# Performance work log

Hardware: AMD Instinct MI355X
Metric: run time of the kernel (lower is better)

## Reference

```python
import jax, jax.numpy as jnp
import numpy as np

BATCH, SEQ, D_IN, D_H = 128, 256, 1024, 1024


def setup_inputs() -> dict:
    key = jax.random.key(0)
    k = jax.random.split(key, 5)
    s = 0.02  # small init scale, like trained weights
    return {
        "x": jax.random.normal(k[0], (BATCH, SEQ, D_IN), dtype=jnp.float32),
        "W0": jax.random.normal(k[1], (3, D_IN + D_H, D_H), dtype=jnp.float32) * s,
        "b0": jax.random.normal(k[2], (3, D_H), dtype=jnp.float32) * s,
        "W1": jax.random.normal(k[3], (3, 2 * D_H, D_H), dtype=jnp.float32) * s,
        "b1": jax.random.normal(k[4], (3, D_H), dtype=jnp.float32) * s,
    }


def _cell(x, h, W, b):
    # non-standard GRU cell: f,i from concat(x,h); z from concat(x, h*i)
    cat = jnp.concatenate([x, h], axis=-1)            # [B, in+H]
    f = jax.nn.sigmoid(cat @ W[0] + b[0])             # forget-like gate
    i = jax.nn.sigmoid(cat @ W[1] + b[1])             # input gate on h
    z = jnp.tanh(jnp.concatenate([x, h * i], axis=-1) @ W[2] + b[2])
    return (1.0 - f) * h + f * z


def reference(x, W0, b0, W1, b1):
    sg = jax.lax.stop_gradient
    batch = x.shape[0]
    h0 = jnp.zeros((batch, D_H), dtype=x.dtype)

    def step(h, x_t):
        h = _cell(x_t, sg(h), W0, b0)                 # first layer (h detached)
        h = _cell(sg(h), sg(h), W1, b1)               # hidden layer (both detached); dropout p=0 -> identity
        return h, None

    xs = jnp.swapaxes(x, 0, 1)                        # [T, B, D_in]
    h_final, _ = jax.lax.scan(step, h0, xs)
    return h_final
```

## Files before the change

### kernel.cpp

```cpp
#include <hip/hip_runtime.h>

#define BB    128
#define TSEQ  256
#define DH    1024
#define DK2   2048
#define NWG   256
#define NTHR  512

typedef __attribute__((ext_vector_type(8))) short short8;
typedef __attribute__((ext_vector_type(4))) float f32x4;

__device__ __forceinline__ unsigned short f2bf(float f) {
    union { float f; unsigned int u; } v; v.f = f;
    unsigned int r = (v.u + 0x7FFFu + ((v.u >> 16) & 1u)) >> 16;
    return (unsigned short)r;
}

__device__ __forceinline__ int imin2(int a, int b) { return a < b ? a : b; }

#define MFMA(a, b, c) __builtin_amdgcn_mfma_f32_16x16x32_bf16((a), (b), (c), 0, 0, 0)

__device__ __forceinline__ void cstoref(float* p, float v) {
    asm volatile("global_store_dword %0, %1, off sc0 sc1" :: "v"(p), "v"(v) : "memory");
}
__device__ __forceinline__ void cstoreh(unsigned short* p, unsigned short v) {
    unsigned int w = v;
    asm volatile("global_store_short %0, %1, off sc0 sc1" :: "v"(p), "v"(w) : "memory");
}

template<int INV>
__device__ __forceinline__ void gbar(int* bar, int lg, int wg) {
    asm volatile("s_waitcnt vmcnt(0)" ::: "memory");
    __syncthreads();
    const int tid = threadIdx.x;
    if (tid == 0) {
        int* fp = bar + wg * 16;
        int v = lg + 1;
        asm volatile("global_store_dword %0, %1, off sc0 sc1" :: "v"(fp), "v"(v) : "memory");
    }
    if (tid < 64) {
        const int* f0 = bar + (tid +   0) * 16;
        const int* f1 = bar + (tid +  64) * 16;
        const int* f2 = bar + (tid + 128) * 16;
        const int* f3 = bar + (tid + 192) * 16;
        const int target = lg + 1;
        for (;;) {
            int a, b, c, d;
            asm volatile("global_load_dword %0, %1, off sc0 sc1" : "=v"(a) : "v"(f0) : "memory");
            asm volatile("global_load_dword %0, %1, off sc0 sc1" : "=v"(b) : "v"(f1) : "memory");
            asm volatile("global_load_dword %0, %1, off sc0 sc1" : "=v"(c) : "v"(f2) : "memory");
            asm volatile("global_load_dword %0, %1, off sc0 sc1" : "=v"(d) : "v"(f3) : "memory");
            asm volatile("s_waitcnt vmcnt(0)" ::: "memory");
            int m = imin2(imin2(a, b), imin2(c, d));
            #pragma unroll
            for (int off = 32; off >= 1; off >>= 1)
                m = imin2(m, __shfl_xor(m, off, 64));
            if (__builtin_amdgcn_readfirstlane(m) >= target) break;
            __builtin_amdgcn_s_sleep(1);
        }
        if (INV) __builtin_amdgcn_fence(__ATOMIC_ACQUIRE, "agent");
    }
    __syncthreads();
}

__global__ __launch_bounds__(256) void prep_weights(const float* __restrict__ W0,
                                                    const float* __restrict__ W1,
                                                    unsigned short* W0f, unsigned short* W0i,
                                                    unsigned short* W0z, unsigned short* Wff,
                                                    unsigned short* Wii, unsigned short* W1z,
                                                    float* h, unsigned short* hb,
                                                    int* bar) {
    int job = blockIdx.x;
    if (job >= 10240) {
        int i0 = (job - 10240) * 2048 + threadIdx.x;
        #pragma unroll
        for (int k = 0; k < 8; ++k) { int i = i0 + k * 256; h[i] = 0.f; hb[i] = 0; }
        return;
    }
    if (job == 0) {
        for (int i = threadIdx.x; i < 4096; i += 256) bar[i] = 0;
    }
    __shared__ float tl[32][33];
    const int tx = threadIdx.x & 31, ty = threadIdx.x >> 5;
    if (job < 6144) {
        int g = job >> 11, r = job & 2047, kt = r >> 5, nt = r & 31;
        const float* src = W0 + (size_t)g * DK2 * DH;
        unsigned short* dst = (g == 0) ? W0f : ((g == 1) ? W0i : W0z);
        #pragma unroll
        for (int i = 0; i < 4; ++i)
            tl[ty + i * 8][tx] = src[(size_t)(kt * 32 + ty + i * 8) * DH + nt * 32 + tx];
        __syncthreads();
        #pragma unroll
        for (int i = 0; i < 4; ++i)
            dst[(size_t)(nt * 32 + ty + i * 8) * DK2 + kt * 32 + tx] = f2bf(tl[tx][ty + i * 8]);
    } else if (job < 8192) {
        int r = job - 6144; int g = r >> 10; r &= 1023;
        int kt = r >> 5, nt = r & 31;
        const float* src = W1 + (size_t)g * DK2 * DH;
        unsigned short* dst = (g == 0) ? Wff : Wii;
        #pragma unroll
        for (int i = 0; i < 4; ++i)
            tl[ty + i * 8][tx] = src[(size_t)(kt * 32 + ty + i * 8) * DH + nt * 32 + tx]
                               + src[(size_t)(1024 + kt * 32 + ty + i * 8) * DH + nt * 32 + tx];
        __syncthreads();
        #pragma unroll
        for (int i = 0; i < 4; ++i)
            dst[(size_t)(nt * 32 + ty + i * 8) * DH + kt * 32 + tx] = f2bf(tl[tx][ty + i * 8]);
    } else {
        int r = job - 8192; int kt = r >> 5, nt = r & 31;
        const float* src = W1 + (size_t)2 * DK2 * DH;
        #pragma unroll
        for (int i = 0; i < 4; ++i)
            tl[ty + i * 8][tx] = src[(size_t)(kt * 32 + ty + i * 8) * DH + nt * 32 + tx];
        __syncthreads();
        #pragma unroll
        for (int i = 0; i < 4; ++i)
            W1z[(size_t)(nt * 32 + ty + i * 8) * DK2 + kt * 32 + tx] = f2bf(tl[tx][ty + i * 8]);
    }
}

struct GruParams {
    const float* x;
    const float* b0;
    const float* b1;
    const unsigned short* W0f;
    const unsigned short* W0i;
    const unsigned short* W0z;
    const unsigned short* Wff;
    const unsigned short* Wii;
    const unsigned short* W1z;
    float* xpre;
    float* h;  unsigned short* hb;
    float* fg;
    unsigned short* hib;
    float* h1;
    unsigned short* hcat;
    float* f2g;
    float* out;
    int* bar;
};

__global__ __launch_bounds__(NTHR) void gru_main(GruParams P) {
    const int wg   = blockIdx.x;
    const int xcd  = wg & 7;
    const int sub  = wg >> 3;
    const int tid  = threadIdx.x;
    const int lane = tid & 63;
    const int wv   = tid >> 6;
    const int tile = wv & 3, ks2 = wv >> 2;
    const int cw   = wv & 1, ks4 = wv >> 1;
    const int lr   = lane & 15;
    const int kb   = (lane >> 4) * 8;
    const int drow = (lane >> 4) * 4;

    __shared__ float s_red[4][16][17];
    __shared__ float s_r2[2][3][16][17];

    int lg = 0;
    const int band = xcd * 128;

    for (int t = 0; t < TSEQ; ++t) {
        if ((t & 31) == 0) {
            for (int j = sub; j < 192; j += 32) {
                int mb = j / 6, cj = j % 6;
                int g = cj >> 1, off = (cj & 1) * 64;
                int col0 = band + off;
                int b = wv * 16 + lr;
                const float* xp = P.x + ((size_t)b * TSEQ + (t + mb)) * DH + kb;
                const unsigned short* wt = (g == 0) ? P.W0f : ((g == 1) ? P.W0i : P.W0z);
                const unsigned short* wp = wt + (size_t)(col0 + lr) * DK2 + kb;
                f32x4 a0 = {0,0,0,0}, a1 = a0, a2 = a0, a3 = a0;
                #pragma unroll 2
                for (int k = 0; k < DH; k += 32) {
                    f32x4 lo = *(const f32x4*)(xp + k);
                    f32x4 hi = *(const f32x4*)(xp + k + 4);
                    short8 av;
                    av[0] = (short)f2bf(lo[0]); av[1] = (short)f2bf(lo[1]);
                    av[2] = (short)f2bf(lo[2]); av[3] = (short)f2bf(lo[3]);
                    av[4] = (short)f2bf(hi[0]); av[5] = (short)f2bf(hi[1]);
                    av[6] = (short)f2bf(hi[2]); av[7] = (short)f2bf(hi[3]);
                    short8 b0v = *(const short8*)(wp + k);
                    short8 b1v = *(const short8*)(wp + (size_t)16 * DK2 + k);
                    short8 b2v = *(const short8*)(wp + (size_t)32 * DK2 + k);
                    short8 b3v = *(const short8*)(wp + (size_t)48 * DK2 + k);
                    a0 = MFMA(av, b0v, a0);
                    a1 = MFMA(av, b1v, a1);
                    a2 = MFMA(av, b2v, a2);
                    a3 = MFMA(av, b3v, a3);
                }
                int rowb = mb * 128 + wv * 16 + drow;
                #pragma unroll
                for (int cf = 0; cf < 4; ++cf) {
                    f32x4 acc = (cf == 0) ? a0 : ((cf == 1) ? a1 : ((cf == 2) ? a2 : a3));
                    int col = g * DH + col0 + cf * 16 + lr;
                    #pragma unroll
                    for (int rr = 0; rr < 4; ++rr)
                        cstoref(P.xpre + (size_t)(rowb + rr) * 3072 + col, acc[rr]);
                }
            }
            gbar<0>(P.bar, lg, wg); ++lg;
        }
        const int tq = t & 31;

        {
            int gate = sub >> 4, rem = sub & 15;
            int mb = rem >> 2, nbq = rem & 3;
            const unsigned short* wt = gate ? P.W0i : P.W0f;
            int wm = tile >> 1, wn = tile & 1;
            int rowb = mb * 32 + wm * 16, colb = band + nbq * 32 + wn * 16;
            const unsigned short* ap = P.hb + (size_t)(rowb + lr) * DH + ks2 * 512 + kb;
            const unsigned short* wp = wt + (size_t)(colb + lr) * DK2 + 1024 + ks2 * 512 + kb;
            int n = colb + lr;
            short8 a[16];
            #pragma unroll
            for (int k = 0; k < 16; ++k) a[k] = *(const short8*)(ap + (size_t)k * 32);
            float xv[4] = {0,0,0,0}, hv[4] = {0,0,0,0};
            if (ks2 == 0) {
                #pragma unroll
                for (int rr = 0; rr < 4; ++rr)
                    xv[rr] = P.xpre[(size_t)(tq * 128 + rowb + drow + rr) * 3072 + gate * DH + n];
                if (gate == 1) {
                    #pragma unroll
                    for (int rr = 0; rr < 4; ++rr)
                        hv[rr] = P.h[(size_t)(rowb + drow + rr) * DH + n];
                }
            }
            short8 bw[16];
            #pragma unroll
            for (int k = 0; k < 16; ++k) bw[k] = *(const short8*)(wp + (size_t)k * 32);
            f32x4 acc = {0.f, 0.f, 0.f, 0.f};
            #pragma unroll
            for (int k = 0; k < 16; ++k) acc = MFMA(a[k], bw[k], acc);
            if (ks2 == 1) {
                s_red[tile][drow + 0][lr] = acc[0]; s_red[tile][drow + 1][lr] = acc[1];
                s_red[tile][drow + 2][lr] = acc[2]; s_red[tile][drow + 3][lr] = acc[3];
            }
            __syncthreads();
            if (ks2 == 0) {
                acc[0] += s_red[tile][drow + 0][lr]; acc[1] += s_red[tile][drow + 1][lr];
                acc[2] += s_red[tile][drow + 2][lr]; acc[3] += s_red[tile][drow + 3][lr];
                float bias = P.b0[gate * DH + n];
                #pragma unroll
                for (int rr = 0; rr < 4; ++rr) {
                    int b = rowb + drow + rr;
                    float pre = acc[rr] + xv[rr] + bias;
                    float s = 1.f / (1.f + __expf(-pre));
                    if (gate == 0) cstoref(P.fg + (size_t)b * DH + n, s);
                    else           cstoreh(P.hib + (size_t)b * DH + n, f2bf(hv[rr] * s));
                }
            }
            gbar<0>(P.bar, lg, wg); ++lg;
        }

        {
            int rowb = (sub >> 2) * 16, colb = band + (sub & 3) * 32 + cw * 16;
            const unsigned short* ap = P.hib + (size_t)(rowb + lr) * DH + ks4 * 256 + kb;
            const unsigned short* wp = P.W0z + (size_t)(colb + lr) * DK2 + 1024 + ks4 * 256 + kb;
            int n = colb + lr;
            short8 a[8];
            #pragma unroll
            for (int k = 0; k < 8; ++k) a[k] = *(const short8*)(ap + (size_t)k * 32);
            float xv[4] = {0,0,0,0}, fv[4] = {0,0,0,0}, hv[4] = {0,0,0,0};
            if (ks4 == 0) {
                #pragma unroll
                for (int rr = 0; rr < 4; ++rr) {
                    int b = rowb + drow + rr;
                    xv[rr] = P.xpre[(size_t)(tq * 128 + b) * 3072 + 2 * DH + n];
                    fv[rr] = P.fg[(size_t)b * DH + n];
                    hv[rr] = P.h[(size_t)b * DH + n];
                }
            }
            short8 bw[8];
            #pragma unroll
            for (int k = 0; k < 8; ++k) bw[k] = *(const short8*)(wp + (size_t)k * 32);
            f32x4 acc = {0.f, 0.f, 0.f, 0.f};
            #pragma unroll
            for (int k = 0; k < 8; ++k) acc = MFMA(a[k], bw[k], acc);
            if (ks4 != 0) {
                s_r2[cw][ks4 - 1][drow + 0][lr] = acc[0]; s_r2[cw][ks4 - 1][drow + 1][lr] = acc[1];
                s_r2[cw][ks4 - 1][drow + 2][lr] = acc[2]; s_r2[cw][ks4 - 1][drow + 3][lr] = acc[3];
            }
            __syncthreads();
            if (ks4 == 0) {
                #pragma unroll
                for (int rr = 0; rr < 4; ++rr)
                    acc[rr] += s_r2[cw][0][drow + rr][lr] + s_r2[cw][1][drow + rr][lr]
                             + s_r2[cw][2][drow + rr][lr];
                float bias = P.b0[2 * DH + n];
                #pragma unroll
                for (int rr = 0; rr < 4; ++rr) {
                    int b = rowb + drow + rr;
                    float pre = acc[rr] + xv[rr] + bias;
                    float z = tanhf(pre);
                    float nh = (1.f - fv[rr]) * hv[rr] + fv[rr] * z;
                    cstoref(P.h1 + (size_t)b * DH + n, nh);
                    cstoreh(P.hcat + (size_t)b * DK2 + n, f2bf(nh));
                }
            }
            gbar<0>(P.bar, lg, wg); ++lg;
        }

        {
            int gate = sub >> 4, rem = sub & 15;
            int mb = rem >> 2, nbq = rem & 3;
            const unsigned short* wt = gate ? P.Wii : P.Wff;
            int wm = tile >> 1, wn = tile & 1;
            int rowb = mb * 32 + wm * 16, colb = band + nbq * 32 + wn * 16;
            const unsigned short* ap = P.hcat + (size_t)(rowb + lr) * DK2 + ks2 * 512 + kb;
            const unsigned short* wp = wt + (size_t)(colb + lr) * DH + ks2 * 512 + kb;
            int n = colb + lr;
            short8 a[16];
            #pragma unroll
            for (int k = 0; k < 16; ++k) a[k] = *(const short8*)(ap + (size_t)k * 32);
            float h1v[4] = {0,0,0,0};
            if (ks2 == 0 && gate == 1) {
                #pragma unroll
                for (int rr = 0; rr < 4; ++rr)
                    h1v[rr] = P.h1[(size_t)(rowb + drow + rr) * DH + n];
            }
            short8 bw[16];
            #pragma unroll
            for (int k = 0; k < 16; ++k) bw[k] = *(const short8*)(wp + (size_t)k * 32);
            f32x4 acc = {0.f, 0.f, 0.f, 0.f};
            #pragma unroll
            for (int k = 0; k < 16; ++k) acc = MFMA(a[k], bw[k], acc);
            if (ks2 == 1) {
                s_red[tile][drow + 0][lr] = acc[0]; s_red[tile][drow + 1][lr] = acc[1];
                s_red[tile][drow + 2][lr] = acc[2]; s_red[tile][drow + 3][lr] = acc[3];
            }
            __syncthreads();
            if (ks2 == 0) {
                acc[0] += s_red[tile][drow + 0][lr]; acc[1] += s_red[tile][drow + 1][lr];
                acc[2] += s_red[tile][drow + 2][lr]; acc[3] += s_red[tile][drow + 3][lr];
                float bias = P.b1[gate * DH + n];
                #pragma unroll
                for (int rr = 0; rr < 4; ++rr) {
                    int b = rowb + drow + rr;
                    float pre = acc[rr] + bias;
                    float s = 1.f / (1.f + __expf(-pre));
                    if (gate == 0) cstoref(P.f2g + (size_t)b * DH + n, s);
                    else           cstoreh(P.hcat + (size_t)b * DK2 + DH + n, f2bf(h1v[rr] * s));
                }
            }
            gbar<0>(P.bar, lg, wg); ++lg;
        }

        {
            int rowb = (sub >> 2) * 16, colb = band + (sub & 3) * 32 + cw * 16;
            const unsigned short* ap = P.hcat + (size_t)(rowb + lr) * DK2 + ks4 * 512 + kb;
            const unsigned short* wp = P.W1z + (size_t)(colb + lr) * DK2 + ks4 * 512 + kb;
            int n = colb + lr;
            short8 a[16];
            #pragma unroll
            for (int k = 0; k < 16; ++k) a[k] = *(const short8*)(ap + (size_t)k * 32);
            float f2v[4] = {0,0,0,0}, h1v[4] = {0,0,0,0};
            if (ks4 == 0) {
                #pragma unroll
                for (int rr = 0; rr < 4; ++rr) {
                    int b = rowb + drow + rr;
                    f2v[rr] = P.f2g[(size_t)b * DH + n];
                    h1v[rr] = P.h1[(size_t)b * DH + n];
                }
            }
            short8 bw[16];
            #pragma unroll
            for (int k = 0; k < 16; ++k) bw[k] = *(const short8*)(wp + (size_t)k * 32);
            f32x4 acc = {0.f, 0.f, 0.f, 0.f};
            #pragma unroll
            for (int k = 0; k < 16; ++k) acc = MFMA(a[k], bw[k], acc);
            if (ks4 != 0) {
                s_r2[cw][ks4 - 1][drow + 0][lr] = acc[0]; s_r2[cw][ks4 - 1][drow + 1][lr] = acc[1];
                s_r2[cw][ks4 - 1][drow + 2][lr] = acc[2]; s_r2[cw][ks4 - 1][drow + 3][lr] = acc[3];
            }
            __syncthreads();
            if (ks4 == 0) {
                #pragma unroll
                for (int rr = 0; rr < 4; ++rr)
                    acc[rr] += s_r2[cw][0][drow + rr][lr] + s_r2[cw][1][drow + rr][lr]
                             + s_r2[cw][2][drow + rr][lr];
                float bias = P.b1[2 * DH + n];
                #pragma unroll
                for (int rr = 0; rr < 4; ++rr) {
                    int b = rowb + drow + rr;
                    float pre = acc[rr] + bias;
                    float z = tanhf(pre);
                    float nh = (1.f - f2v[rr]) * h1v[rr] + f2v[rr] * z;
                    cstoref(P.h + (size_t)b * DH + n, nh);
                    cstoreh(P.hb + (size_t)b * DH + n, f2bf(nh));
                    if (t == TSEQ - 1) P.out[(size_t)b * DH + n] = nh;
                }
            }
            gbar<1>(P.bar, lg, wg); ++lg;
        }
    }
}

extern "C" void kernel_launch(void* const* d_in, const int* in_sizes, int n_in,
                              void* d_out, int out_size, void* d_ws, size_t ws_size,
                              hipStream_t stream) {
    const float* x  = (const float*)d_in[0];
    const float* W0 = (const float*)d_in[1];
    const float* b0 = (const float*)d_in[2];
    const float* W1 = (const float*)d_in[3];
    const float* b1 = (const float*)d_in[4];

    char* ws = (char*)d_ws;
    size_t off = 0;
    auto alloc = [&](size_t bytes) { void* p = ws + off; off += (bytes + 255) & ~(size_t)255; return p; };

    unsigned short* W0f = (unsigned short*)alloc((size_t)DH * DK2 * 2);
    unsigned short* W0i = (unsigned short*)alloc((size_t)DH * DK2 * 2);
    unsigned short* W0z = (unsigned short*)alloc((size_t)DH * DK2 * 2);
    unsigned short* W1z = (unsigned short*)alloc((size_t)DH * DK2 * 2);
    unsigned short* Wff = (unsigned short*)alloc((size_t)DH * DH * 2);
    unsigned short* Wii = (unsigned short*)alloc((size_t)DH * DH * 2);
    float* xpre = (float*)alloc((size_t)32 * 128 * 3072 * 4);
    float* h    = (float*)alloc((size_t)BB * DH * 4);
    unsigned short* hb = (unsigned short*)alloc((size_t)BB * DH * 2);
    float* fg   = (float*)alloc((size_t)BB * DH * 4);
    unsigned short* hib = (unsigned short*)alloc((size_t)BB * DH * 2);
    float* h1   = (float*)alloc((size_t)BB * DH * 4);
    unsigned short* hcat = (unsigned short*)alloc((size_t)BB * DK2 * 2);
    float* f2g  = (float*)alloc((size_t)BB * DH * 4);
    int* bar    = (int*)alloc(16384);
    (void)ws_size; (void)in_sizes; (void)n_in; (void)out_size;

    prep_weights<<<10304, 256, 0, stream>>>(W0, W1, W0f, W0i, W0z, Wff, Wii, W1z,
                                            h, hb, bar);

    GruParams p;
    p.x = x; p.b0 = b0; p.b1 = b1;
    p.W0f = W0f; p.W0i = W0i; p.W0z = W0z; p.Wff = Wff; p.Wii = Wii; p.W1z = W1z;
    p.xpre = xpre; p.h = h; p.hb = hb; p.fg = fg; p.hib = hib;
    p.h1 = h1; p.hcat = hcat; p.f2g = f2g;
    p.out = (float*)d_out;
    p.bar = bar;

    void* args[] = { &p };
    hipLaunchCooperativeKernel((const void*)gru_main, dim3(NWG), dim3(NTHR), args, 0, stream);
}
```

Measured before the change: 11.62 ms.

## Split batch into independent WG clusters with per-cluster grid barriers

```diff
diff --git a/kernel.cpp b/kernel.cpp
--- a/kernel.cpp
+++ b/kernel.cpp
@@ -39,19 +39,13 @@
         asm volatile("global_store_dword %0, %1, off sc0 sc1" :: "v"(fp), "v"(v) : "memory");
     }
     if (tid < 64) {
-        const int* f0 = bar + (tid +   0) * 16;
-        const int* f1 = bar + (tid +  64) * 16;
-        const int* f2 = bar + (tid + 128) * 16;
-        const int* f3 = bar + (tid + 192) * 16;
+        const int* f0 = bar + ((wg >> 6) * 64 + tid) * 16;
         const int target = lg + 1;
         for (;;) {
-            int a, b, c, d;
+            int a;
             asm volatile("global_load_dword %0, %1, off sc0 sc1" : "=v"(a) : "v"(f0) : "memory");
-            asm volatile("global_load_dword %0, %1, off sc0 sc1" : "=v"(b) : "v"(f1) : "memory");
-            asm volatile("global_load_dword %0, %1, off sc0 sc1" : "=v"(c) : "v"(f2) : "memory");
-            asm volatile("global_load_dword %0, %1, off sc0 sc1" : "=v"(d) : "v"(f3) : "memory");
             asm volatile("s_waitcnt vmcnt(0)" ::: "memory");
-            int m = imin2(imin2(a, b), imin2(c, d));
+            int m = a;
             #pragma unroll
             for (int off = 32; off >= 1; off >>= 1)
                 m = imin2(m, __shfl_xor(m, off, 64));
@@ -142,8 +136,8 @@
 
 __global__ __launch_bounds__(NTHR) void gru_main(GruParams P) {
     const int wg   = blockIdx.x;
-    const int xcd  = wg & 7;
-    const int sub  = wg >> 3;
+    const int c    = wg >> 6;
+    const int cwg  = wg & 63;
     const int tid  = threadIdx.x;
     const int lane = tid & 63;
     const int wv   = tid >> 6;
@@ -157,18 +151,21 @@
     __shared__ float s_r2[2][3][16][17];
 
     int lg = 0;
-    const int band = xcd * 128;
+    const int crow = c * 32;
+
+    const int gateAC = cwg >> 5, nctAC = cwg & 31;
+    const int rhBD   = cwg >> 5, nctBD = cwg & 31;
 
     for (int t = 0; t < TSEQ; ++t) {
         if ((t & 31) == 0) {
-            for (int j = sub; j < 192; j += 32) {
-                int mb = j / 6, cj = j % 6;
-                int g = cj >> 1, off = (cj & 1) * 64;
-                int col0 = band + off;
-                int b = wv * 16 + lr;
-                const float* xp = P.x + ((size_t)b * TSEQ + (t + mb)) * DH + kb;
+            for (int j = cwg; j < 384; j += 64) {
+                int tt = j / 12, cj = j % 12;
+                int g = cj >> 2;
+                int gcol0 = (cj & 3) * 256 + (wv & 3) * 64;
+                int b = crow + (wv >> 2) * 16 + lr;
+                const float* xp = P.x + ((size_t)b * TSEQ + (t + tt)) * DH + kb;
                 const unsigned short* wt = (g == 0) ? P.W0f : ((g == 1) ? P.W0i : P.W0z);
-                const unsigned short* wp = wt + (size_t)(col0 + lr) * DK2 + kb;
+                const unsigned short* wp = wt + (size_t)(gcol0 + lr) * DK2 + kb;
                 f32x4 a0 = {0,0,0,0}, a1 = a0, a2 = a0, a3 = a0;
                 #pragma unroll 2
                 for (int k = 0; k < DH; k += 32) {
@@ -188,11 +185,11 @@
                     a2 = MFMA(av, b2v, a2);
                     a3 = MFMA(av, b3v, a3);
                 }
-                int rowb = mb * 128 + wv * 16 + drow;
+                int rowb = tt * 128 + crow + (wv >> 2) * 16 + drow;
                 #pragma unroll
                 for (int cf = 0; cf < 4; ++cf) {
                     f32x4 acc = (cf == 0) ? a0 : ((cf == 1) ? a1 : ((cf == 2) ? a2 : a3));
-                    int col = g * DH + col0 + cf * 16 + lr;
+                    int col = g * DH + gcol0 + cf * 16 + lr;
                     #pragma unroll
                     for (int rr = 0; rr < 4; ++rr)
                         cstoref(P.xpre + (size_t)(rowb + rr) * 3072 + col, acc[rr]);
@@ -203,11 +200,10 @@
         const int tq = t & 31;
 
         {
-            int gate = sub >> 4, rem = sub & 15;
-            int mb = rem >> 2, nbq = rem & 3;
+            const int gate = gateAC;
             const unsigned short* wt = gate ? P.W0i : P.W0f;
             int wm = tile >> 1, wn = tile & 1;
-            int rowb = mb * 32 + wm * 16, colb = band + nbq * 32 + wn * 16;
+            int rowb = crow + wm * 16, colb = nctAC * 32 + wn * 16;
             const unsigned short* ap = P.hb + (size_t)(rowb + lr) * DH + ks2 * 512 + kb;
             const unsigned short* wp = wt + (size_t)(colb + lr) * DK2 + 1024 + ks2 * 512 + kb;
             int n = colb + lr;
@@ -253,7 +249,7 @@
         }
 
         {
-            int rowb = (sub >> 2) * 16, colb = band + (sub & 3) * 32 + cw * 16;
+            int rowb = crow + rhBD * 16, colb = nctBD * 32 + cw * 16;
             const unsigned short* ap = P.hib + (size_t)(rowb + lr) * DH + ks4 * 256 + kb;
             const unsigned short* wp = P.W0z + (size_t)(colb + lr) * DK2 + 1024 + ks4 * 256 + kb;
             int n = colb + lr;
@@ -301,11 +297,10 @@
         }
 
         {
-            int gate = sub >> 4, rem = sub & 15;
-            int mb = rem >> 2, nbq = rem & 3;
+            const int gate = gateAC;
             const unsigned short* wt = gate ? P.Wii : P.Wff;
             int wm = tile >> 1, wn = tile & 1;
-            int rowb = mb * 32 + wm * 16, colb = band + nbq * 32 + wn * 16;
+            int rowb = crow + wm * 16, colb = nctAC * 32 + wn * 16;
             const unsigned short* ap = P.hcat + (size_t)(rowb + lr) * DK2 + ks2 * 512 + kb;
             const unsigned short* wp = wt + (size_t)(colb + lr) * DH + ks2 * 512 + kb;
             int n = colb + lr;
@@ -346,7 +341,7 @@
         }
 
         {
-            int rowb = (sub >> 2) * 16, colb = band + (sub & 3) * 32 + cw * 16;
+            int rowb = crow + rhBD * 16, colb = nctBD * 32 + cw * 16;
             const unsigned short* ap = P.hcat + (size_t)(rowb + lr) * DK2 + ks4 * 512 + kb;
             const unsigned short* wp = P.W1z + (size_t)(colb + lr) * DK2 + ks4 * 512 + kb;
             int n = colb + lr;
```

Result: faster. 11.21 ms, median of 4 (-3.5%).
